# Performance work log

Measured on AMD Instinct MI355X. Metric: run time of the kernel, lower is better.

The kernel has to match this reference:

```python
import jax, jax.numpy as jnp
import numpy as np

DIM = 1024
CROSS_DIM = 768
NUM_HEADS = 16
HEAD_DIM = DIM // NUM_HEADS
B, S, SC = 4, 2048, 1024


def setup_inputs() -> dict:
    key = jax.random.key(0)
    ks = jax.random.split(key, 12)
    x = jax.random.normal(ks[0], (B, S, DIM), dtype=jnp.float32)
    cross_x = jax.random.normal(ks[1], (B, SC, CROSS_DIM), dtype=jnp.float32)
    # ragged cross lengths -> padding mask (True = ignore)
    lengths = jax.random.randint(ks[2], (B,), SC // 2, SC + 1)
    key_padding_mask = jnp.arange(SC)[None, :] >= lengths[:, None]  # (B, SC) bool
    s = 0.02
    Wq = jax.random.normal(ks[3], (DIM, DIM), dtype=jnp.float32) * s
    bq = jnp.zeros((DIM,), dtype=jnp.float32)
    Wk = jax.random.normal(ks[4], (CROSS_DIM, DIM), dtype=jnp.float32) * s
    bk = jnp.zeros((DIM,), dtype=jnp.float32)
    Wv = jax.random.normal(ks[5], (CROSS_DIM, DIM), dtype=jnp.float32) * s
    bv = jnp.zeros((DIM,), dtype=jnp.float32)
    Wo = jax.random.normal(ks[6], (DIM, DIM), dtype=jnp.float32) * s
    bo = jnp.zeros((DIM,), dtype=jnp.float32)
    return {"x": x, "cross_x": cross_x, "key_padding_mask": key_padding_mask,
            "Wq": Wq, "bq": bq, "Wk": Wk, "bk": bk, "Wv": Wv, "bv": bv,
            "Wo": Wo, "bo": bo}


def reference(x, cross_x, key_padding_mask, Wq, bq, Wk, bk, Wv, bv, Wo, bo):
    b, s, _ = x.shape
    sc = cross_x.shape[1]
    # projections (torch Linear: x @ W + b with W stored as (in, out) here)
    q = (x @ Wq + bq).reshape(b, s, NUM_HEADS, HEAD_DIM).transpose(0, 2, 1, 3)
    k = (cross_x @ Wk + bk).reshape(b, sc, NUM_HEADS, HEAD_DIM).transpose(0, 2, 1, 3)
    v = (cross_x @ Wv + bv).reshape(b, sc, NUM_HEADS, HEAD_DIM).transpose(0, 2, 1, 3)
    # (b, h, s, sc) attention scores
    scores = jnp.einsum('bhsd,bhcd->bhsc', q, k) / jnp.sqrt(jnp.float32(HEAD_DIM))
    mask = key_padding_mask[:, None, None, :]  # (b,1,1,sc), True = ignore
    scores = jnp.where(mask, -jnp.inf, scores)
    # original subtracts row max then softmax; equivalent stable softmax
    scores = scores - jnp.max(scores, axis=-1, keepdims=True)
    attn = jax.nn.softmax(scores, axis=-1)
    out = jnp.einsum('bhsc,bhcd->bhsd', attn, v)
    out = out.transpose(0, 2, 1, 3).reshape(b, s, DIM)
    return out @ Wo + bo
```

## Files before the change

### kernel.cpp

```cpp
#include <hip/hip_runtime.h>
#include <hip/hip_bf16.h>
#include <stdint.h>

#define DIM_ 1024
#define NH_ 16
#define HD_ 64
#define B_ 4
#define S_ 2048
#define SC_ 1024
#define CD_ 768

typedef __attribute__((ext_vector_type(8))) short bf16x8;
typedef __attribute__((ext_vector_type(4))) short bf16x4;
typedef __attribute__((ext_vector_type(4))) float f32x4;

__device__ inline unsigned short f2bf(float f) {
    __hip_bfloat16 h = __float2bfloat16(f);
    return __builtin_bit_cast(unsigned short, h);
}

#define GLOAD16(SRC, DST) __builtin_amdgcn_global_load_lds( \
    (const __attribute__((address_space(1))) void*)(SRC),   \
    (__attribute__((address_space(3))) void*)(DST), 16, 0, 0)

__global__ void k_f32_to_bf16(const float* __restrict__ in, unsigned short* __restrict__ out, int n4) {
    int i = blockIdx.x * blockDim.x + threadIdx.x;
    int stride = gridDim.x * blockDim.x;
    for (; i < n4; i += stride) {
        float4 v = ((const float4*)in)[i];
        uint2 pk;
        pk.x = (unsigned int)f2bf(v.x) | ((unsigned int)f2bf(v.y) << 16);
        pk.y = (unsigned int)f2bf(v.z) | ((unsigned int)f2bf(v.w) << 16);
        ((uint2*)out)[i] = pk;
    }
}

__global__ void k_transposeW(const float* __restrict__ W, unsigned short* __restrict__ WT, int K) {
    int idx = blockIdx.x * blockDim.x + threadIdx.x;
    if (idx >= (K >> 3) * 1024) return;
    int n = idx & 1023;
    int k0 = (idx >> 10) << 3;
    unsigned int pk[4];
#pragma unroll
    for (int j = 0; j < 4; ++j) {
        unsigned short a = f2bf(W[(size_t)(k0 + 2 * j) * 1024 + n]);
        unsigned short b = f2bf(W[(size_t)(k0 + 2 * j + 1) * 1024 + n]);
        pk[j] = (unsigned int)a | ((unsigned int)b << 16);
    }
    *(uint4*)&WT[(size_t)n * K + k0] = *(uint4*)pk;
}

__global__ void k_mask_bits(const unsigned int* __restrict__ m,
                            unsigned int* __restrict__ bits, int* __restrict__ ntp) {
    __shared__ int bm_s;
    __shared__ unsigned int wbits[128];
    if (threadIdx.x == 0) bm_s = 0;
    __syncthreads();
    int any = 0;
    for (int i = threadIdx.x; i < 1024; i += 256)
        if (m[i] > 1u) any = 1;
    if (any) atomicOr(&bm_s, 1);
    __syncthreads();
    const int boolmode = bm_s;
    const int w = threadIdx.x;
    if (w < 128) {
        const unsigned char* mb = (const unsigned char*)m;
        unsigned int out = 0;
        for (int j = 0; j < 32; ++j) {
            int c = w * 32 + j;
            int masked = boolmode ? (mb[c] != 0) : (m[c] != 0u);
            out |= (unsigned int)masked << j;
        }
        bits[w] = out;
        wbits[w] = out;
    }
    __syncthreads();
    if (threadIdx.x < 4) {
        int nt = 0;
        for (int tt = 0; tt < 16; ++tt) {
            unsigned int w0 = wbits[threadIdx.x * 32 + tt * 2];
            unsigned int w1 = wbits[threadIdx.x * 32 + tt * 2 + 1];
            if ((w0 & w1) != 0xFFFFFFFFu) nt = tt + 1;
        }
        ntp[threadIdx.x] = nt;
    }
}

template<int EPI>
__global__ __launch_bounds__(256) void k_gemm_bt(
    const unsigned short* __restrict__ A, const unsigned short* __restrict__ BT,
    const float* __restrict__ bias, const float* __restrict__ bias2, float oscale,
    unsigned short* __restrict__ Cb, unsigned short* __restrict__ Cb2,
    float* __restrict__ Cf, int M, int N, int K)
{
    __shared__ unsigned short As[2][128 * 32];
    __shared__ unsigned short Bs[2][128 * 32];
    const int t = threadIdx.x;
    const int w = t >> 6, lane = t & 63;
    const int lo = lane & 15, hi = lane >> 4;
    const int nwg = gridDim.x * gridDim.y;
    const int wg = blockIdx.y * gridDim.x + blockIdx.x;
    const int swz = (wg & 7) * (nwg >> 3) + (wg >> 3);
    const int m0 = (swz % gridDim.x) * 128, n0 = (swz / gridDim.x) * 128;
    const int wr = (w >> 1) * 64, wc = (w & 1) * 64;
    const int srow = lane >> 2;
    const int scol = (lane & 3) * 8;

    f32x4 zero4 = {0.f, 0.f, 0.f, 0.f};
    f32x4 acc[4][4];
    for (int i = 0; i < 4; ++i)
        for (int j = 0; j < 4; ++j) acc[i][j] = zero4;

#pragma unroll
    for (int p = 0; p < 2; ++p) {
        int chunk = w * 2 + p;
        int r = chunk * 16 + srow;
        GLOAD16(&A[(size_t)(m0 + r) * K + scol], &As[0][chunk * 512]);
        GLOAD16(&BT[(size_t)(n0 + r) * K + scol], &Bs[0][chunk * 512]);
    }
    __syncthreads();

    int cur = 0;
    for (int k0 = 0; k0 < K; k0 += 32) {
        if (k0 + 32 < K) {
#pragma unroll
            for (int p = 0; p < 2; ++p) {
                int chunk = w * 2 + p;
                int r = chunk * 16 + srow;
                GLOAD16(&A[(size_t)(m0 + r) * K + k0 + 32 + scol], &As[cur ^ 1][chunk * 512]);
                GLOAD16(&BT[(size_t)(n0 + r) * K + k0 + 32 + scol], &Bs[cur ^ 1][chunk * 512]);
            }
        }
        bf16x8 af[4], bfr[4];
#pragma unroll
        for (int i = 0; i < 4; ++i)
            af[i] = *(const bf16x8*)&As[cur][(wr + i * 16 + lo) * 32 + (hi << 3)];
#pragma unroll
        for (int j = 0; j < 4; ++j)
            bfr[j] = *(const bf16x8*)&Bs[cur][(wc + j * 16 + lo) * 32 + (hi << 3)];
#pragma unroll
        for (int i = 0; i < 4; ++i)
#pragma unroll
            for (int j = 0; j < 4; ++j)
                acc[i][j] = __builtin_amdgcn_mfma_f32_16x16x32_bf16(af[i], bfr[j], acc[i][j], 0, 0, 0);
        __syncthreads();
        cur ^= 1;
    }

#pragma unroll
    for (int i = 0; i < 4; ++i) {
#pragma unroll
        for (int j = 0; j < 4; ++j) {
#pragma unroll
            for (int r = 0; r < 4; ++r) {
                int m = m0 + wr + i * 16 + (hi << 2) + r;
                int n = n0 + wc + j * 16 + lo;
                if (EPI == 0) {
                    float v = (acc[i][j][r] + bias[n]) * oscale;
                    Cb[(size_t)m * 1024 + n] = f2bf(v);
                } else if (EPI == 2) {
                    float v = (acc[i][j][r] + bias[n]) * oscale;
                    Cf[(size_t)m * 1024 + n] = v;
                } else if (EPI == 3) {
                    if (n < 1024) {
                        float v = acc[i][j][r] + bias[n];
                        Cb[(size_t)m * 1024 + n] = f2bf(v);
                    } else {
                        float v = acc[i][j][r] + bias2[n - 1024];
                        int bb = m >> 10, c = m & 1023;
                        Cb2[(size_t)((bb << 10) + (n - 1024)) * 1024 + c] = f2bf(v);
                    }
                }
            }
        }
    }
}

__global__ __launch_bounds__(256) void k_attn(
    const unsigned short* __restrict__ Q, const unsigned short* __restrict__ Kb,
    const unsigned short* __restrict__ VT, const unsigned int* __restrict__ bits,
    const int* __restrict__ ntp, unsigned short* __restrict__ Ob)
{
    __shared__ unsigned short lds[16384];
    const int t = threadIdx.x, w = t >> 6, lane = t & 63;
    const int lo = lane & 15, hi = lane >> 4;
    const int qt = blockIdx.x, h = blockIdx.y, b = blockIdx.z;
    const int qr0 = qt * 128 + w * 32;
    const int l7 = lo & 7;
    const int nt = ntp[b];

    const int srow = lane >> 3;
    const int scb  = ((lane & 7) ^ srow) << 3;

    bf16x8 qf[2][2];
#pragma unroll
    for (int qh = 0; qh < 2; ++qh)
#pragma unroll
        for (int kk = 0; kk < 2; ++kk)
            qf[qh][kk] = *(const bf16x8*)&Q[(size_t)(b * S_ + qr0 + qh * 16 + lo) * DIM_ + h * 64 + kk * 32 + hi * 8];

    f32x4 zero4 = {0.f, 0.f, 0.f, 0.f};
    float mrow[2] = {-1e30f, -1e30f}, lsum[2] = {0.f, 0.f};
    f32x4 o[4][2];
#pragma unroll
    for (int dt = 0; dt < 4; ++dt)
#pragma unroll
        for (int qh = 0; qh < 2; ++qh) o[dt][qh] = zero4;

#pragma unroll
    for (int s = 0; s < 2; ++s) {
        int rl = w * 16 + s * 8 + srow;
        GLOAD16(&Kb[(size_t)(b * SC_ + rl) * DIM_ + h * 64 + scb], &lds[(w * 16 + s * 8) * 64]);
        GLOAD16(&VT[(size_t)(b * 1024 + h * 64 + rl) * SC_ + scb], &lds[8192 + (w * 16 + s * 8) * 64]);
    }
    __syncthreads();

    int cur = 0;
    for (int tt = 0; tt < nt; ++tt) {
        if (tt + 1 < nt) {
            int c0n = (tt + 1) * 64;
#pragma unroll
            for (int s = 0; s < 2; ++s) {
                int rl = w * 16 + s * 8 + srow;
                GLOAD16(&Kb[(size_t)(b * SC_ + c0n + rl) * DIM_ + h * 64 + scb],
                        &lds[(cur ^ 1) * 4096 + (w * 16 + s * 8) * 64]);
                GLOAD16(&VT[(size_t)(b * 1024 + h * 64 + rl) * SC_ + c0n + scb],
                        &lds[8192 + (cur ^ 1) * 4096 + (w * 16 + s * 8) * 64]);
            }
        }
        const unsigned short* Kl = &lds[cur * 4096];
        const unsigned short* Vl = &lds[8192 + cur * 4096];

        f32x4 st[4][2];
#pragma unroll
        for (int n = 0; n < 4; ++n)
#pragma unroll
            for (int qh = 0; qh < 2; ++qh) st[n][qh] = zero4;
#pragma unroll
        for (int n = 0; n < 4; ++n) {
            const int R = n * 16 + lo;
            bf16x8 k0 = *(const bf16x8*)&Kl[R * 64 + ((hi ^ l7) << 3)];
            bf16x8 k1 = *(const bf16x8*)&Kl[R * 64 + (((4 + hi) ^ l7) << 3)];
#pragma unroll
            for (int qh = 0; qh < 2; ++qh) {
                st[n][qh] = __builtin_amdgcn_mfma_f32_16x16x32_bf16(k0, qf[qh][0], st[n][qh], 0, 0, 0);
                st[n][qh] = __builtin_amdgcn_mfma_f32_16x16x32_bf16(k1, qf[qh][1], st[n][qh], 0, 0, 0);
            }
        }
        bf16x4 vf[4][4];
#pragma unroll
        for (int dt = 0; dt < 4; ++dt)
#pragma unroll
            for (int n = 0; n < 4; ++n)
                vf[dt][n] = *(const bf16x4*)&Vl[(dt * 16 + lo) * 64
                              + (((2 * n + (hi >> 1)) ^ l7) << 3) + ((hi & 1) << 2)];

        uint2 mw = *(const uint2*)&bits[b * 32 + tt * 2];

        float p[2][4][4];
        float mx[2] = {-1e30f, -1e30f};
        if ((mw.x | mw.y) == 0u) {
#pragma unroll
            for (int n = 0; n < 4; ++n)
#pragma unroll
                for (int r = 0; r < 4; ++r)
#pragma unroll
                    for (int qh = 0; qh < 2; ++qh) {
                        float s = st[n][qh][r];
                        p[qh][n][r] = s;
                        mx[qh] = fmaxf(mx[qh], s);
                    }
        } else {
#pragma unroll
            for (int n = 0; n < 4; ++n) {
                unsigned int wd = (n & 2) ? mw.y : mw.x;
#pragma unroll
                for (int r = 0; r < 4; ++r) {
                    int sh = ((n & 1) << 4) + (hi << 2) + r;
                    bool mk = (wd >> sh) & 1u;
#pragma unroll
                    for (int qh = 0; qh < 2; ++qh) {
                        float s = mk ? -1e30f : st[n][qh][r];
                        p[qh][n][r] = s;
                        mx[qh] = fmaxf(mx[qh], s);
                    }
                }
            }
        }
        float m2[2];
#pragma unroll
        for (int qh = 0; qh < 2; ++qh) {
            float v = fmaxf(mx[qh], __shfl_xor(mx[qh], 16));
            m2[qh] = fmaxf(v, __shfl_xor(v, 32));
        }
        float growth = fmaxf(m2[0] - mrow[0], m2[1] - mrow[1]);
        if (!__all(growth <= 8.0f)) {
#pragma unroll
            for (int qh = 0; qh < 2; ++qh) {
                float mnew = fmaxf(mrow[qh], m2[qh]);
                float scl = __builtin_amdgcn_exp2f(mrow[qh] - mnew);
                mrow[qh] = mnew;
                lsum[qh] *= scl;
#pragma unroll
                for (int dt = 0; dt < 4; ++dt)
#pragma unroll
                    for (int r = 0; r < 4; ++r)
                        o[dt][qh][r] *= scl;
            }
        }
#pragma unroll
        for (int qh = 0; qh < 2; ++qh) {
            float rs = 0.f;
#pragma unroll
            for (int n = 0; n < 4; ++n)
#pragma unroll
                for (int r = 0; r < 4; ++r) {
                    float e = __builtin_amdgcn_exp2f(p[qh][n][r] - mrow[qh]);
                    p[qh][n][r] = e;
                    rs += e;
                }
            rs += __shfl_xor(rs, 16);
            rs += __shfl_xor(rs, 32);
            lsum[qh] += rs;
        }
#pragma unroll
        for (int qh = 0; qh < 2; ++qh) {
#pragma unroll
            for (int n = 0; n < 4; ++n) {
                uint2 pk2;
                pk2.x = (unsigned int)f2bf(p[qh][n][0]) | ((unsigned int)f2bf(p[qh][n][1]) << 16);
                pk2.y = (unsigned int)f2bf(p[qh][n][2]) | ((unsigned int)f2bf(p[qh][n][3]) << 16);
                bf16x4 pb = __builtin_bit_cast(bf16x4, pk2);
#pragma unroll
                for (int dt = 0; dt < 4; ++dt)
                    o[dt][qh] = __builtin_amdgcn_mfma_f32_16x16x16bf16_1k(vf[dt][n], pb, o[dt][qh], 0, 0, 0);
            }
        }
        __syncthreads();
        cur ^= 1;
    }

    unsigned short* Tl = &lds[w * 2304];
    float inv[2] = {1.0f / lsum[0], 1.0f / lsum[1]};
#pragma unroll
    for (int qh = 0; qh < 2; ++qh)
#pragma unroll
        for (int dt = 0; dt < 4; ++dt)
#pragma unroll
            for (int r = 0; r < 4; ++r)
                Tl[(qh * 16 + lo) * 72 + dt * 16 + hi * 4 + r] = f2bf(o[dt][qh][r] * inv[qh]);
#pragma unroll
    for (int ps = 0; ps < 4; ++ps) {
        int row = ps * 8 + (lane >> 3);
        int col = (lane & 7) * 8;
        bf16x8 v = *(const bf16x8*)&Tl[row * 72 + col];
        *(bf16x8*)&Ob[(size_t)(b * S_ + qr0 + row) * DIM_ + h * 64 + col] = v;
    }
}

extern "C" void kernel_launch(void* const* d_in, const int* in_sizes, int n_in,
                              void* d_out, int out_size, void* d_ws, size_t ws_size,
                              hipStream_t stream)
{
    const float* x  = (const float*)d_in[0];
    const float* cx = (const float*)d_in[1];
    const void* mask = d_in[2];
    const float* Wq = (const float*)d_in[3];
    const float* bq = (const float*)d_in[4];
    const float* Wk = (const float*)d_in[5];
    const float* bk = (const float*)d_in[6];
    const float* Wv = (const float*)d_in[7];
    const float* bv = (const float*)d_in[8];
    const float* Wo = (const float*)d_in[9];
    const float* bo = (const float*)d_in[10];

    unsigned short* ws = (unsigned short*)d_ws;
    const size_t XB  = 0;
    const size_t CXB = XB  + (size_t)8192 * 1024;
    const size_t WQT = CXB + (size_t)4096 * 768;
    const size_t WKT = WQT + (size_t)1024 * 1024;
    const size_t WVT = WKT + (size_t)1024 * 768;
    const size_t WOT = WVT + (size_t)1024 * 768;
    const size_t QB  = WOT + (size_t)1024 * 1024;
    const size_t KB  = QB  + (size_t)8192 * 1024;
    const size_t VTB = KB  + (size_t)4096 * 1024;
    const size_t MBT = VTB + (size_t)4 * 1024 * 1024;
    const size_t NTP = MBT + 256;

    k_f32_to_bf16<<<2048, 256, 0, stream>>>(x,  ws + XB,  8192 * 1024 / 4);
    k_f32_to_bf16<<<2048, 256, 0, stream>>>(cx, ws + CXB, 4096 * 768 / 4);
    k_transposeW<<<512, 256, 0, stream>>>(Wq, ws + WQT, 1024);
    k_transposeW<<<384, 256, 0, stream>>>(Wk, ws + WKT, 768);
    k_transposeW<<<384, 256, 0, stream>>>(Wv, ws + WVT, 768);
    k_transposeW<<<512, 256, 0, stream>>>(Wo, ws + WOT, 1024);
    unsigned int* mbits = (unsigned int*)(ws + MBT);
    int* ntp = (int*)(ws + NTP);
    k_mask_bits<<<1, 256, 0, stream>>>((const unsigned int*)mask, mbits, ntp);

    const float QSCALE = 0.125f * 1.44269504088896340736f;
    dim3 gq(8192 / 128, 1024 / 128);
    dim3 gkv(4096 / 128, 2048 / 128);
    k_gemm_bt<0><<<gq, 256, 0, stream>>>(ws + XB, ws + WQT, bq, nullptr, QSCALE, ws + QB, nullptr, nullptr, 8192, 1024, 1024);
    k_gemm_bt<3><<<gkv, 256, 0, stream>>>(ws + CXB, ws + WKT, bk, bv, 1.0f, ws + KB, ws + VTB, nullptr, 4096, 2048, 768);

    dim3 ga(S_ / 128, NH_, B_);
    k_attn<<<ga, 256, 0, stream>>>(ws + QB, ws + KB, ws + VTB, mbits, ntp, ws + XB);

    k_gemm_bt<2><<<gq, 256, 0, stream>>>(ws + XB, ws + WOT, bo, nullptr, 1.0f, nullptr, nullptr, (float*)d_out, 8192, 1024, 1024);
}
```

Measured before the change: 187.6 us.

## Merge weight transposes, vectorize V-transpose epilogue stores, vectorize softmax max/sum

Combines the four weight transpose/convert launches into one kernel that dispatches on thread index, removing three launches. In the K/V projection GEMM epilogue, the transposed V output is now written as packed 4-element bf16 stores instead of scalar 2-byte scatters. The attention softmax computes the row max and the exp sum with f32x4 vector ops in a tree reduction, and rescales the accumulators as vectors. Together these cut launch overhead, store transactions and serial dependency chains, at the cost of some added index branching in the transpose kernel.

```diff
diff --git a/kernel.cpp b/kernel.cpp
--- a/kernel.cpp
+++ b/kernel.cpp
@@ -17,6 +17,13 @@
 __device__ inline unsigned short f2bf(float f) {
     __hip_bfloat16 h = __float2bfloat16(f);
     return __builtin_bit_cast(unsigned short, h);
+}
+
+__device__ inline f32x4 vmax4(f32x4 a, f32x4 b) {
+    f32x4 r;
+#pragma unroll
+    for (int i = 0; i < 4; ++i) r[i] = fmaxf(a[i], b[i]);
+    return r;
 }
 
 #define GLOAD16(SRC, DST) __builtin_amdgcn_global_load_lds( \
@@ -35,9 +42,16 @@
     }
 }
 
-__global__ void k_transposeW(const float* __restrict__ W, unsigned short* __restrict__ WT, int K) {
+__global__ void k_transposeW4(const float* __restrict__ Wq, const float* __restrict__ Wk,
+                              const float* __restrict__ Wv, const float* __restrict__ Wo,
+                              unsigned short* __restrict__ WQT, unsigned short* __restrict__ WKT,
+                              unsigned short* __restrict__ WVT, unsigned short* __restrict__ WOT) {
     int idx = blockIdx.x * blockDim.x + threadIdx.x;
-    if (idx >= (K >> 3) * 1024) return;
+    const float* W; unsigned short* WT; int K;
+    if (idx < 131072)      { W = Wq; WT = WQT; K = 1024; }
+    else if (idx < 229376) { W = Wk; WT = WKT; K = 768;  idx -= 131072; }
+    else if (idx < 327680) { W = Wv; WT = WVT; K = 768;  idx -= 229376; }
+    else                   { W = Wo; WT = WOT; K = 1024; idx -= 327680; }
     int n = idx & 1023;
     int k0 = (idx >> 10) << 3;
     unsigned int pk[4];
@@ -151,24 +165,28 @@
     for (int i = 0; i < 4; ++i) {
 #pragma unroll
         for (int j = 0; j < 4; ++j) {
-#pragma unroll
-            for (int r = 0; r < 4; ++r) {
-                int m = m0 + wr + i * 16 + (hi << 2) + r;
-                int n = n0 + wc + j * 16 + lo;
-                if (EPI == 0) {
-                    float v = (acc[i][j][r] + bias[n]) * oscale;
-                    Cb[(size_t)m * 1024 + n] = f2bf(v);
-                } else if (EPI == 2) {
-                    float v = (acc[i][j][r] + bias[n]) * oscale;
-                    Cf[(size_t)m * 1024 + n] = v;
-                } else if (EPI == 3) {
-                    if (n < 1024) {
+            int n = n0 + wc + j * 16 + lo;
+            int mbase = m0 + wr + i * 16 + (hi << 2);
+            if (EPI == 3 && n >= 1024) {
+                float b2 = bias2[n - 1024];
+                uint2 pk;
+                pk.x = (unsigned int)f2bf(acc[i][j][0] + b2) | ((unsigned int)f2bf(acc[i][j][1] + b2) << 16);
+                pk.y = (unsigned int)f2bf(acc[i][j][2] + b2) | ((unsigned int)f2bf(acc[i][j][3] + b2) << 16);
+                int bb = mbase >> 10, c = mbase & 1023;
+                *(uint2*)&Cb2[(size_t)((bb << 10) + (n - 1024)) * 1024 + c] = pk;
+            } else {
+#pragma unroll
+                for (int r = 0; r < 4; ++r) {
+                    int m = mbase + r;
+                    if (EPI == 0) {
+                        float v = (acc[i][j][r] + bias[n]) * oscale;
+                        Cb[(size_t)m * 1024 + n] = f2bf(v);
+                    } else if (EPI == 2) {
+                        float v = (acc[i][j][r] + bias[n]) * oscale;
+                        Cf[(size_t)m * 1024 + n] = v;
+                    } else {
                         float v = acc[i][j][r] + bias[n];
                         Cb[(size_t)m * 1024 + n] = f2bf(v);
-                    } else {
-                        float v = acc[i][j][r] + bias2[n - 1024];
-                        int bb = m >> 10, c = m & 1023;
-                        Cb2[(size_t)((bb << 10) + (n - 1024)) * 1024 + c] = f2bf(v);
                     }
                 }
             }
@@ -257,20 +275,18 @@
 
         uint2 mw = *(const uint2*)&bits[b * 32 + tt * 2];
 
-        float p[2][4][4];
-        float mx[2] = {-1e30f, -1e30f};
+        f32x4 p[2][4];
+        float mx[2];
         if ((mw.x | mw.y) == 0u) {
 #pragma unroll
-            for (int n = 0; n < 4; ++n)
-#pragma unroll
-                for (int r = 0; r < 4; ++r)
-#pragma unroll
-                    for (int qh = 0; qh < 2; ++qh) {
-                        float s = st[n][qh][r];
-                        p[qh][n][r] = s;
-                        mx[qh] = fmaxf(mx[qh], s);
-                    }
+            for (int qh = 0; qh < 2; ++qh) {
+                f32x4 a = vmax4(vmax4(st[0][qh], st[1][qh]), vmax4(st[2][qh], st[3][qh]));
+                mx[qh] = fmaxf(fmaxf(a[0], a[1]), fmaxf(a[2], a[3]));
+#pragma unroll
+                for (int n = 0; n < 4; ++n) p[qh][n] = st[n][qh];
+            }
         } else {
+            mx[0] = -1e30f; mx[1] = -1e30f;
 #pragma unroll
             for (int n = 0; n < 4; ++n) {
                 unsigned int wd = (n & 2) ? mw.y : mw.x;
@@ -303,22 +319,22 @@
                 lsum[qh] *= scl;
 #pragma unroll
                 for (int dt = 0; dt < 4; ++dt)
-#pragma unroll
-                    for (int r = 0; r < 4; ++r)
-                        o[dt][qh][r] *= scl;
+                    o[dt][qh] *= scl;
             }
         }
 #pragma unroll
         for (int qh = 0; qh < 2; ++qh) {
-            float rs = 0.f;
-#pragma unroll
-            for (int n = 0; n < 4; ++n)
-#pragma unroll
-                for (int r = 0; r < 4; ++r) {
-                    float e = __builtin_amdgcn_exp2f(p[qh][n][r] - mrow[qh]);
-                    p[qh][n][r] = e;
-                    rs += e;
-                }
+            f32x4 rs4 = zero4;
+#pragma unroll
+            for (int n = 0; n < 4; ++n) {
+                f32x4 e;
+#pragma unroll
+                for (int r = 0; r < 4; ++r)
+                    e[r] = __builtin_amdgcn_exp2f(p[qh][n][r] - mrow[qh]);
+                p[qh][n] = e;
+                rs4 += e;
+            }
+            float rs = (rs4[0] + rs4[1]) + (rs4[2] + rs4[3]);
             rs += __shfl_xor(rs, 16);
             rs += __shfl_xor(rs, 32);
             lsum[qh] += rs;
@@ -389,10 +405,7 @@
 
     k_f32_to_bf16<<<2048, 256, 0, stream>>>(x,  ws + XB,  8192 * 1024 / 4);
     k_f32_to_bf16<<<2048, 256, 0, stream>>>(cx, ws + CXB, 4096 * 768 / 4);
-    k_transposeW<<<512, 256, 0, stream>>>(Wq, ws + WQT, 1024);
-    k_transposeW<<<384, 256, 0, stream>>>(Wk, ws + WKT, 768);
-    k_transposeW<<<384, 256, 0, stream>>>(Wv, ws + WVT, 768);
-    k_transposeW<<<512, 256, 0, stream>>>(Wo, ws + WOT, 1024);
+    k_transposeW4<<<1792, 256, 0, stream>>>(Wq, Wk, Wv, Wo, ws + WQT, ws + WKT, ws + WVT, ws + WOT);
     unsigned int* mbits = (unsigned int*)(ws + MBT);
     int* ntp = (int*)(ws + NTP);
     k_mask_bits<<<1, 256, 0, stream>>>((const unsigned int*)mask, mbits, ntp);
```

After: 170.7 us. 1.1x faster.
